# Kernel tuning notes

Hardware: AMD Instinct MI355X
Metric: run time of the kernel (lower is better)

Reference implementation:

```python
import jax, jax.numpy as jnp
import numpy as np

LN_EPS = 1e-5  # torch LayerNorm default

def _lnorm(x):
    # LayerNorm over last dim, no affine params
    mu = jnp.mean(x, axis=-1, keepdims=True)
    var = jnp.var(x, axis=-1, keepdims=True)
    return (x - mu) / jnp.sqrt(var + LN_EPS)

def setup_inputs() -> dict:
    key = jax.random.key(0)
    k0, k1, k2, k3 = jax.random.split(key, 4)
    B, S, D, H = 4, 4096, 1024, 64
    xs_q = jax.random.normal(k0, (B, S, D), dtype=jnp.float32)
    # torch Linear(D, H, bias=False) stores weight [H, D]; we store [D, H] = W.T
    sc = 1.0 / np.sqrt(D)
    Wq = jax.random.normal(k1, (D, H), dtype=jnp.float32) * sc
    Wk = jax.random.normal(k2, (D, H), dtype=jnp.float32) * sc
    Wv = jax.random.normal(k3, (D, H), dtype=jnp.float32) * sc
    return {"xs_q": xs_q, "Wq": Wq, "Wk": Wk, "Wv": Wv}

def reference(xs_q, Wq, Wk, Wv):
    # self-attention: xs_k_v = xs_q
    qs = _lnorm(jnp.einsum('bsd,dh->bsh', xs_q, Wq))  # [B,S,H]
    ks = _lnorm(jnp.einsum('bsd,dh->bsh', xs_q, Wk))
    vs = jnp.einsum('bsd,dh->bsh', xs_q, Wv)
    scaling = 1.0 / jnp.sqrt(jnp.asarray(qs.shape[-1], dtype=qs.dtype))
    att = jnp.einsum('bqh,bkh->bqk', qs, ks)          # [B,S,S] full attention matrix
    probs = jax.nn.softmax(scaling * att, axis=-1)
    vsp = jnp.einsum('bqk,bkh->bqh', probs, vs)       # [B,S,H]
    return vsp
```

## Files before the change

### kernel.cpp

```cpp
#include <hip/hip_runtime.h>
#include <hip/hip_bf16.h>


typedef __bf16 bf16x8 __attribute__((ext_vector_type(8)));
typedef __bf16 bf16x4 __attribute__((ext_vector_type(4)));
typedef short s16x4 __attribute__((ext_vector_type(4)));
typedef float f32x4 __attribute__((ext_vector_type(4)));

#define NROW 16384
#define DD   1024
#define HH   64
#define SS   4096
#define LS   68

#if __has_builtin(__builtin_amdgcn_mfma_f32_16x16x16_bf16)
#define MFMA16(a, b, c) __builtin_amdgcn_mfma_f32_16x16x16_bf16((a), (b), (c), 0, 0, 0)
#define HAVE_MFMA16 1
#elif __has_builtin(__builtin_amdgcn_mfma_f32_16x16x16bf16_1k)
#define MFMA16(a, b, c)                                             \
  __builtin_amdgcn_mfma_f32_16x16x16bf16_1k(                        \
      __builtin_bit_cast(s16x4, (a)), __builtin_bit_cast(s16x4, (b)), (c), 0, 0, 0)
#define HAVE_MFMA16 1
#endif

static __device__ inline unsigned short f2bf_u(float x) {
  __bf16 b = (__bf16)x;
  return __builtin_bit_cast(unsigned short, b);
}
static __device__ inline uint2 pk4f(float a, float b, float c, float d) {
  return make_uint2((unsigned)f2bf_u(a) | ((unsigned)f2bf_u(b) << 16),
                    (unsigned)f2bf_u(c) | ((unsigned)f2bf_u(d) << 16));
}
static __device__ inline bf16x8 ld8(const __bf16* p) {
  bf16x4 lo = *reinterpret_cast<const bf16x4*>(p);
  bf16x4 hi = *reinterpret_cast<const bf16x4*>(p + 4);
  return __builtin_shufflevector(lo, hi, 0, 1, 2, 3, 4, 5, 6, 7);
}

__global__ __launch_bounds__(256) void k_transpose_w(
    const float* __restrict__ Wq, const float* __restrict__ Wk,
    const float* __restrict__ Wv, __bf16* __restrict__ WT) {
  int idx = blockIdx.x * 256 + threadIdx.x;
  int mat = idx >> 16;
  int rem = idx & 65535;
  int k = rem >> 6, h = rem & 63;
  const float* W = (mat == 0) ? Wq : ((mat == 1) ? Wk : Wv);
  WT[(size_t)(mat * 64 + h) * DD + k] = (__bf16)W[rem];
}

__global__ __launch_bounds__(128, 2) void k_proj(
    const float* __restrict__ X, const __bf16* __restrict__ WT,
    __bf16* __restrict__ qb, __bf16* __restrict__ kbp, __bf16* __restrict__ vT) {
  __shared__ __bf16 Xs[32 * LS];
  __shared__ __bf16 Ws[192 * LS];
  const int t = threadIdx.x, lane = t & 63, w = t >> 6;
  const int quad = lane >> 4, m = lane & 15;
  const int Mb = blockIdx.x * 32;

  f32x4 acc[12];
#pragma unroll
  for (int i = 0; i < 12; i++) acc[i] = (f32x4){0.f, 0.f, 0.f, 0.f};

  float4 xr[4];
  bf16x8 wr[12];
#pragma unroll
  for (int i = 0; i < 4; i++) {
    int c = t + i * 128, row = c >> 4, col = (c & 15) * 4;
    xr[i] = *reinterpret_cast<const float4*>(&X[(size_t)(Mb + row) * DD + col]);
  }
#pragma unroll
  for (int i = 0; i < 12; i++) {
    int c = t + i * 128, row = c >> 3, col = (c & 7) * 8;
    wr[i] = *reinterpret_cast<const bf16x8*>(&WT[(size_t)row * DD + col]);
  }

  for (int s = 0; s < 16; s++) {
    if (s) __syncthreads();
#pragma unroll
    for (int i = 0; i < 4; i++) {
      int c = t + i * 128, row = c >> 4, col = (c & 15) * 4;
      *reinterpret_cast<uint2*>(&Xs[row * LS + col]) =
          pk4f(xr[i].x, xr[i].y, xr[i].z, xr[i].w);
    }
#pragma unroll
    for (int i = 0; i < 12; i++) {
      int c = t + i * 128, row = c >> 3, col = (c & 7) * 8;
      uint4 raw = __builtin_bit_cast(uint4, wr[i]);
      __bf16* wd = &Ws[row * LS + col];
      *reinterpret_cast<uint2*>(wd) = make_uint2(raw.x, raw.y);
      *reinterpret_cast<uint2*>(wd + 4) = make_uint2(raw.z, raw.w);
    }
    __syncthreads();
    if (s + 1 < 16) {
      const int ko = (s + 1) * 64;
#pragma unroll
      for (int i = 0; i < 4; i++) {
        int c = t + i * 128, row = c >> 4, col = (c & 15) * 4;
        xr[i] = *reinterpret_cast<const float4*>(
            &X[(size_t)(Mb + row) * DD + ko + col]);
      }
#pragma unroll
      for (int i = 0; i < 12; i++) {
        int c = t + i * 128, row = c >> 3, col = (c & 7) * 8;
        wr[i] = *reinterpret_cast<const bf16x8*>(
            &WT[(size_t)row * DD + ko + col]);
      }
    }
#pragma unroll
    for (int kk = 0; kk < 2; kk++) {
      bf16x8 a = ld8(&Xs[(16 * w + m) * LS + 32 * kk + quad * 8]);
#pragma unroll
      for (int nt = 0; nt < 12; nt++) {
        bf16x8 bfr = ld8(&Ws[(16 * nt + m) * LS + 32 * kk + quad * 8]);
        acc[nt] = __builtin_amdgcn_mfma_f32_16x16x32_bf16(a, bfr, acc[nt], 0, 0, 0);
      }
    }
  }

#pragma unroll
  for (int mat = 0; mat < 2; mat++) {
#pragma unroll
    for (int reg = 0; reg < 4; reg++) {
      float s = 0.f, s2 = 0.f;
#pragma unroll
      for (int ntl = 0; ntl < 4; ntl++) {
        float x = acc[mat * 4 + ntl][reg];
        s += x; s2 += x * x;
      }
#pragma unroll
      for (int off = 1; off < 16; off <<= 1) {
        s += __shfl_xor(s, off, 64);
        s2 += __shfl_xor(s2, off, 64);
      }
      float mu = s * (1.0f / 64.0f);
      float var = s2 * (1.0f / 64.0f) - mu * mu;
      float rstd = rsqrtf(var + 1e-5f);
      float scl = (mat == 0) ? 0.125f * 1.44269504f * rstd : rstd;
#pragma unroll
      for (int ntl = 0; ntl < 4; ntl++)
        acc[mat * 4 + ntl][reg] = (acc[mat * 4 + ntl][reg] - mu) * scl;
    }
  }

  const int rowbase = Mb + 16 * w + quad * 4;
#pragma unroll
  for (int nt = 0; nt < 4; nt++)
#pragma unroll
    for (int reg = 0; reg < 4; reg++) {
      qb[(size_t)(rowbase + reg) * HH + m + 16 * nt] = (__bf16)acc[nt][reg];
      kbp[(size_t)(rowbase + reg) * HH + m + 16 * nt] = (__bf16)acc[4 + nt][reg];
    }
  const int b = Mb >> 12;
  const int s0 = (Mb & 4095) + 16 * w + quad * 4;
#pragma unroll
  for (int nt = 0; nt < 4; nt++) {
    ushort4 pk = make_ushort4(f2bf_u(acc[8 + nt][0]), f2bf_u(acc[8 + nt][1]),
                              f2bf_u(acc[8 + nt][2]), f2bf_u(acc[8 + nt][3]));
    *reinterpret_cast<ushort4*>(
        &vT[((size_t)(b * 64) + m + 16 * nt) * SS + s0]) = pk;
  }
}

__global__ __launch_bounds__(256, 4) void k_attn(
    const __bf16* __restrict__ qb, const __bf16* __restrict__ kbp,
    const __bf16* __restrict__ vT, float* __restrict__ Op,
    float* __restrict__ lp, int spbits) {
  __shared__ __align__(16) char smem[17408];
  __bf16* Klds = (__bf16*)smem;
  __bf16* Vlds = (__bf16*)(smem + 8704);
  const int t = threadIdx.x, lane = t & 63, w = t >> 6;
  const int quad = lane >> 4, m = lane & 15;
  const int wq = w >> 1, wk = w & 1;
  const int nsp = 1 << spbits;
  const int qt = blockIdx.x >> spbits, sp = blockIdx.x & (nsp - 1);
  const int KPS = SS >> spbits;
  const int Mb = qt * 64;
  const int b = Mb >> 12;
  const size_t kvbase = (size_t)b * SS * HH;

  bf16x8 qf[2][2];
#pragma unroll
  for (int ntl = 0; ntl < 2; ntl++)
#pragma unroll
    for (int kk = 0; kk < 2; kk++)
      qf[ntl][kk] = *reinterpret_cast<const bf16x8*>(
          &qb[(size_t)(Mb + (2 * wq + ntl) * 16 + m) * HH + 32 * kk + quad * 8]);

  f32x4 O[4][2];
#pragma unroll
  for (int i = 0; i < 4; i++)
#pragma unroll
    for (int j = 0; j < 2; j++) O[i][j] = (f32x4){0.f, 0.f, 0.f, 0.f};
  float ll[2] = {0.f, 0.f};

  const int c0row = t >> 3, ck0 = (t & 7) * 8;
  const int c1row = c0row + 32;
  const int kb_lo = sp * KPS, kb_hi = kb_lo + KPS;

  uint4 kd0, kd1, vd0, vd1;
  kd0 = *reinterpret_cast<const uint4*>(&kbp[kvbase + (size_t)(kb_lo + c0row) * HH + ck0]);
  kd1 = *reinterpret_cast<const uint4*>(&kbp[kvbase + (size_t)(kb_lo + c1row) * HH + ck0]);
  vd0 = *reinterpret_cast<const uint4*>(&vT[(size_t)(b * 64 + c0row) * SS + kb_lo + ck0]);
  vd1 = *reinterpret_cast<const uint4*>(&vT[(size_t)(b * 64 + c1row) * SS + kb_lo + ck0]);

  for (int kb0 = kb_lo; kb0 < kb_hi; kb0 += 64) {
    {
      __bf16* kp0 = &Klds[c0row * LS + ck0];
      __bf16* kp1 = &Klds[c1row * LS + ck0];
      __bf16* vp0 = &Vlds[c0row * LS + ck0];
      __bf16* vp1 = &Vlds[c1row * LS + ck0];
      *reinterpret_cast<uint2*>(kp0) = make_uint2(kd0.x, kd0.y);
      *reinterpret_cast<uint2*>(kp0 + 4) = make_uint2(kd0.z, kd0.w);
      *reinterpret_cast<uint2*>(kp1) = make_uint2(kd1.x, kd1.y);
      *reinterpret_cast<uint2*>(kp1 + 4) = make_uint2(kd1.z, kd1.w);
      *reinterpret_cast<uint2*>(vp0) = make_uint2(vd0.x, vd0.y);
      *reinterpret_cast<uint2*>(vp0 + 4) = make_uint2(vd0.z, vd0.w);
      *reinterpret_cast<uint2*>(vp1) = make_uint2(vd1.x, vd1.y);
      *reinterpret_cast<uint2*>(vp1 + 4) = make_uint2(vd1.z, vd1.w);
    }
    __syncthreads();
    if (kb0 + 64 < kb_hi) {
      kd0 = *reinterpret_cast<const uint4*>(&kbp[kvbase + (size_t)(kb0 + 64 + c0row) * HH + ck0]);
      kd1 = *reinterpret_cast<const uint4*>(&kbp[kvbase + (size_t)(kb0 + 64 + c1row) * HH + ck0]);
      vd0 = *reinterpret_cast<const uint4*>(&vT[(size_t)(b * 64 + c0row) * SS + kb0 + 64 + ck0]);
      vd1 = *reinterpret_cast<const uint4*>(&vT[(size_t)(b * 64 + c1row) * SS + kb0 + 64 + ck0]);
    }

#pragma unroll
    for (int ktl = 0; ktl < 2; ktl++) {
      const int kt = 2 * wk + ktl;
      f32x4 sc[2];
      sc[0] = (f32x4){0.f, 0.f, 0.f, 0.f};
      sc[1] = (f32x4){0.f, 0.f, 0.f, 0.f};
#pragma unroll
      for (int kk = 0; kk < 2; kk++) {
        bf16x8 kf = ld8(&Klds[(kt * 16 + m) * LS + 32 * kk + quad * 8]);
        sc[0] = __builtin_amdgcn_mfma_f32_16x16x32_bf16(kf, qf[0][kk], sc[0], 0, 0, 0);
        sc[1] = __builtin_amdgcn_mfma_f32_16x16x32_bf16(kf, qf[1][kk], sc[1], 0, 0, 0);
      }
#pragma unroll
      for (int ntl = 0; ntl < 2; ntl++) {
        float p0 = exp2f(sc[ntl][0]), p1 = exp2f(sc[ntl][1]);
        float p2 = exp2f(sc[ntl][2]), p3 = exp2f(sc[ntl][3]);
        ll[ntl] += (p0 + p1) + (p2 + p3);
        bf16x4 pf;
        pf[0] = (__bf16)p0; pf[1] = (__bf16)p1;
        pf[2] = (__bf16)p2; pf[3] = (__bf16)p3;
#ifdef HAVE_MFMA16
#pragma unroll
        for (int ht = 0; ht < 4; ht++) {
          bf16x4 vf = *reinterpret_cast<const bf16x4*>(
              &Vlds[(16 * ht + m) * LS + kt * 16 + quad * 4]);
          O[ht][ntl] = MFMA16(vf, pf, O[ht][ntl]);
        }
#else
        uint2 pd = __builtin_bit_cast(uint2, pf);
        int lo_src = 32 * quad + m, hi_src = 32 * quad + 16 + m;
        unsigned b0 = (unsigned)__shfl((int)pd.x, lo_src, 64);
        unsigned b1 = (unsigned)__shfl((int)pd.y, lo_src, 64);
        unsigned b2 = (unsigned)__shfl((int)pd.x, hi_src, 64);
        unsigned b3 = (unsigned)__shfl((int)pd.y, hi_src, 64);
        uint4 bz = (quad < 2) ? make_uint4(b0, b1, b2, b3)
                              : make_uint4(0u, 0u, 0u, 0u);
        bf16x8 bfrag = __builtin_bit_cast(bf16x8, bz);
#pragma unroll
        for (int ht = 0; ht < 4; ht++) {
          bf16x8 vf = ld8(&Vlds[(16 * ht + m) * LS + kt * 16 + (quad & 1) * 8]);
          O[ht][ntl] =
              __builtin_amdgcn_mfma_f32_16x16x32_bf16(vf, bfrag, O[ht][ntl], 0, 0, 0);
        }
#endif
      }
    }
    __syncthreads();
  }

#pragma unroll
  for (int ntl = 0; ntl < 2; ntl++) {
    ll[ntl] += __shfl_xor(ll[ntl], 16, 64);
    ll[ntl] += __shfl_xor(ll[ntl], 32, 64);
  }

  float* obuf = (float*)smem;
  float* lbuf = (float*)(smem + 16896);
  __syncthreads();
  if (wk == 1) {
#pragma unroll
    for (int ht = 0; ht < 4; ht++)
#pragma unroll
      for (int ntl = 0; ntl < 2; ntl++)
#pragma unroll
        for (int reg = 0; reg < 4; reg++)
          obuf[wq * 2112 + (16 * ht + quad * 4 + reg) * 33 + ntl * 16 + m] =
              O[ht][ntl][reg];
    if (quad == 0) {
      lbuf[(2 * wq + 0) * 16 + m] = ll[0];
      lbuf[(2 * wq + 1) * 16 + m] = ll[1];
    }
  }
  __syncthreads();
  if (wk == 0) {
#pragma unroll
    for (int ht = 0; ht < 4; ht++)
#pragma unroll
      for (int ntl = 0; ntl < 2; ntl++)
#pragma unroll
        for (int reg = 0; reg < 4; reg++)
          O[ht][ntl][reg] +=
              obuf[wq * 2112 + (16 * ht + quad * 4 + reg) * 33 + ntl * 16 + m];
#pragma unroll
    for (int ntl = 0; ntl < 2; ntl++) {
      const int qg = Mb + (2 * wq + ntl) * 16 + m;
      ll[ntl] += lbuf[(2 * wq + ntl) * 16 + m];
#pragma unroll
      for (int ht = 0; ht < 4; ht++) {
        f32x4 v = O[ht][ntl];
        *reinterpret_cast<float4*>(
            &Op[((size_t)sp * NROW + qg) * HH + 16 * ht + 4 * quad]) =
            make_float4(v[0], v[1], v[2], v[3]);
      }
      if (quad == 0) lp[sp * NROW + qg] = ll[ntl];
    }
  }
}

__global__ __launch_bounds__(256) void k_comb(const float* __restrict__ Op,
                                              const float* __restrict__ lp,
                                              float* __restrict__ out, int nsp) {
  int idx = blockIdx.x * 256 + threadIdx.x;
  int row = idx >> 6;
  float o = 0.f, l = 0.f;
  for (int j = 0; j < nsp; j++) {
    o += Op[(size_t)j * NROW * HH + idx];
    l += lp[j * NROW + row];
  }
  out[idx] = o / l;
}

extern "C" void kernel_launch(void* const* d_in, const int* in_sizes, int n_in,
                              void* d_out, int out_size, void* d_ws, size_t ws_size,
                              hipStream_t stream) {
  const float* X  = (const float*)d_in[0];
  const float* Wq = (const float*)d_in[1];
  const float* Wk = (const float*)d_in[2];
  const float* Wv = (const float*)d_in[3];
  float* out = (float*)d_out;
  char* ws = (char*)d_ws;

  __bf16* WT  = (__bf16*)(ws);
  __bf16* qb  = (__bf16*)(ws + (size_t)512 * 1024);
  __bf16* kbp = (__bf16*)(ws + (size_t)2560 * 1024);
  __bf16* vT  = (__bf16*)(ws + (size_t)4608 * 1024);
  float*  Op  = (float*)(ws + (size_t)6656 * 1024);
  const size_t need8 = (size_t)(6656 + 8 * 4096 + 512) * 1024;
  const int spbits = (ws_size >= need8) ? 3 : 2;
  const int nsp = 1 << spbits;
  float* lp = (float*)(ws + (size_t)(6656 + nsp * 4096) * 1024);

  hipLaunchKernelGGL(k_transpose_w, dim3(768), dim3(256), 0, stream, Wq, Wk, Wv, WT);
  hipLaunchKernelGGL(k_proj, dim3(NROW / 32), dim3(128), 0, stream, X, WT, qb, kbp, vT);
  hipLaunchKernelGGL(k_attn, dim3((NROW / 64) * nsp), dim3(256), 0, stream,
                     qb, kbp, vT, Op, lp, spbits);
  hipLaunchKernelGGL(k_comb, dim3(NROW * HH / 256), dim3(256), 0, stream,
                     Op, lp, out, nsp);
}
```

Measured before the change: 160.8 us.

## Repartition warps: split-K in projection, all-keys per warp in attention

```diff
diff --git a/kernel.cpp b/kernel.cpp
--- a/kernel.cpp
+++ b/kernel.cpp
@@ -48,43 +48,46 @@
   WT[(size_t)(mat * 64 + h) * DD + k] = (__bf16)W[rem];
 }
 
-__global__ __launch_bounds__(128, 2) void k_proj(
+__global__ __launch_bounds__(256, 2) void k_proj(
     const float* __restrict__ X, const __bf16* __restrict__ WT,
     __bf16* __restrict__ qb, __bf16* __restrict__ kbp, __bf16* __restrict__ vT) {
-  __shared__ __bf16 Xs[32 * LS];
-  __shared__ __bf16 Ws[192 * LS];
+  __shared__ __align__(16) char smem[30464];
+  __bf16* Xs = (__bf16*)smem;
+  __bf16* Ws = (__bf16*)(smem + 4352);
   const int t = threadIdx.x, lane = t & 63, w = t >> 6;
   const int quad = lane >> 4, m = lane & 15;
+  const int wl = w & 1;
+  const int kh = w >> 1;
   const int Mb = blockIdx.x * 32;
 
   f32x4 acc[12];
 #pragma unroll
   for (int i = 0; i < 12; i++) acc[i] = (f32x4){0.f, 0.f, 0.f, 0.f};
 
-  float4 xr[4];
-  bf16x8 wr[12];
-#pragma unroll
-  for (int i = 0; i < 4; i++) {
-    int c = t + i * 128, row = c >> 4, col = (c & 15) * 4;
+  float4 xr[2];
+  bf16x8 wr[6];
+#pragma unroll
+  for (int i = 0; i < 2; i++) {
+    int c = t + i * 256, row = c >> 4, col = (c & 15) * 4;
     xr[i] = *reinterpret_cast<const float4*>(&X[(size_t)(Mb + row) * DD + col]);
   }
 #pragma unroll
-  for (int i = 0; i < 12; i++) {
-    int c = t + i * 128, row = c >> 3, col = (c & 7) * 8;
+  for (int i = 0; i < 6; i++) {
+    int c = t + i * 256, row = c >> 3, col = (c & 7) * 8;
     wr[i] = *reinterpret_cast<const bf16x8*>(&WT[(size_t)row * DD + col]);
   }
 
   for (int s = 0; s < 16; s++) {
     if (s) __syncthreads();
 #pragma unroll
-    for (int i = 0; i < 4; i++) {
-      int c = t + i * 128, row = c >> 4, col = (c & 15) * 4;
+    for (int i = 0; i < 2; i++) {
+      int c = t + i * 256, row = c >> 4, col = (c & 15) * 4;
       *reinterpret_cast<uint2*>(&Xs[row * LS + col]) =
           pk4f(xr[i].x, xr[i].y, xr[i].z, xr[i].w);
     }
 #pragma unroll
-    for (int i = 0; i < 12; i++) {
-      int c = t + i * 128, row = c >> 3, col = (c & 7) * 8;
+    for (int i = 0; i < 6; i++) {
+      int c = t + i * 256, row = c >> 3, col = (c & 7) * 8;
       uint4 raw = __builtin_bit_cast(uint4, wr[i]);
       __bf16* wd = &Ws[row * LS + col];
       *reinterpret_cast<uint2*>(wd) = make_uint2(raw.x, raw.y);
@@ -94,28 +97,38 @@
     if (s + 1 < 16) {
       const int ko = (s + 1) * 64;
 #pragma unroll
-      for (int i = 0; i < 4; i++) {
-        int c = t + i * 128, row = c >> 4, col = (c & 15) * 4;
+      for (int i = 0; i < 2; i++) {
+        int c = t + i * 256, row = c >> 4, col = (c & 15) * 4;
         xr[i] = *reinterpret_cast<const float4*>(
             &X[(size_t)(Mb + row) * DD + ko + col]);
       }
 #pragma unroll
-      for (int i = 0; i < 12; i++) {
-        int c = t + i * 128, row = c >> 3, col = (c & 7) * 8;
+      for (int i = 0; i < 6; i++) {
+        int c = t + i * 256, row = c >> 3, col = (c & 7) * 8;
         wr[i] = *reinterpret_cast<const bf16x8*>(
             &WT[(size_t)row * DD + ko + col]);
       }
     }
-#pragma unroll
-    for (int kk = 0; kk < 2; kk++) {
-      bf16x8 a = ld8(&Xs[(16 * w + m) * LS + 32 * kk + quad * 8]);
-#pragma unroll
-      for (int nt = 0; nt < 12; nt++) {
-        bf16x8 bfr = ld8(&Ws[(16 * nt + m) * LS + 32 * kk + quad * 8]);
-        acc[nt] = __builtin_amdgcn_mfma_f32_16x16x32_bf16(a, bfr, acc[nt], 0, 0, 0);
-      }
-    }
-  }
+    bf16x8 a = ld8(&Xs[(16 * wl + m) * LS + 32 * kh + quad * 8]);
+#pragma unroll
+    for (int nt = 0; nt < 12; nt++) {
+      bf16x8 bfr = ld8(&Ws[(16 * nt + m) * LS + 32 * kh + quad * 8]);
+      acc[nt] = __builtin_amdgcn_mfma_f32_16x16x32_bf16(a, bfr, acc[nt], 0, 0, 0);
+    }
+  }
+
+  __syncthreads();
+  float* red = (float*)smem;
+  if (kh == 1) {
+#pragma unroll
+    for (int nt = 0; nt < 12; nt++)
+      *reinterpret_cast<f32x4*>(&red[(wl * 64 + lane) * 52 + nt * 4]) = acc[nt];
+  }
+  __syncthreads();
+  if (kh == 1) return;
+#pragma unroll
+  for (int nt = 0; nt < 12; nt++)
+    acc[nt] += *reinterpret_cast<const f32x4*>(&red[(wl * 64 + lane) * 52 + nt * 4]);
 
 #pragma unroll
   for (int mat = 0; mat < 2; mat++) {
@@ -142,7 +155,7 @@
     }
   }
 
-  const int rowbase = Mb + 16 * w + quad * 4;
+  const int rowbase = Mb + 16 * wl + quad * 4;
 #pragma unroll
   for (int nt = 0; nt < 4; nt++)
 #pragma unroll
@@ -151,7 +164,7 @@
       kbp[(size_t)(rowbase + reg) * HH + m + 16 * nt] = (__bf16)acc[4 + nt][reg];
     }
   const int b = Mb >> 12;
-  const int s0 = (Mb & 4095) + 16 * w + quad * 4;
+  const int s0 = (Mb & 4095) + 16 * wl + quad * 4;
 #pragma unroll
   for (int nt = 0; nt < 4; nt++) {
     ushort4 pk = make_ushort4(f2bf_u(acc[8 + nt][0]), f2bf_u(acc[8 + nt][1]),
@@ -170,11 +183,10 @@
   __bf16* Vlds = (__bf16*)(smem + 8704);
   const int t = threadIdx.x, lane = t & 63, w = t >> 6;
   const int quad = lane >> 4, m = lane & 15;
-  const int wq = w >> 1, wk = w & 1;
   const int nsp = 1 << spbits;
   const int qt = blockIdx.x >> spbits, sp = blockIdx.x & (nsp - 1);
   const int KPS = SS >> spbits;
-  const int Mb = qt * 64;
+  const int Mb = qt * 128;
   const int b = Mb >> 12;
   const size_t kvbase = (size_t)b * SS * HH;
 
@@ -184,7 +196,7 @@
 #pragma unroll
     for (int kk = 0; kk < 2; kk++)
       qf[ntl][kk] = *reinterpret_cast<const bf16x8*>(
-          &qb[(size_t)(Mb + (2 * wq + ntl) * 16 + m) * HH + 32 * kk + quad * 8]);
+          &qb[(size_t)(Mb + 32 * w + 16 * ntl + m) * HH + 32 * kk + quad * 8]);
 
   f32x4 O[4][2];
 #pragma unroll
@@ -227,34 +239,38 @@
     }
 
 #pragma unroll
-    for (int ktl = 0; ktl < 2; ktl++) {
-      const int kt = 2 * wk + ktl;
+    for (int ktl = 0; ktl < 4; ktl++) {
+      bf16x8 kf0 = ld8(&Klds[(ktl * 16 + m) * LS + quad * 8]);
+      bf16x8 kf1 = ld8(&Klds[(ktl * 16 + m) * LS + 32 + quad * 8]);
       f32x4 sc[2];
       sc[0] = (f32x4){0.f, 0.f, 0.f, 0.f};
       sc[1] = (f32x4){0.f, 0.f, 0.f, 0.f};
 #pragma unroll
-      for (int kk = 0; kk < 2; kk++) {
-        bf16x8 kf = ld8(&Klds[(kt * 16 + m) * LS + 32 * kk + quad * 8]);
-        sc[0] = __builtin_amdgcn_mfma_f32_16x16x32_bf16(kf, qf[0][kk], sc[0], 0, 0, 0);
-        sc[1] = __builtin_amdgcn_mfma_f32_16x16x32_bf16(kf, qf[1][kk], sc[1], 0, 0, 0);
-      }
+      for (int ntl = 0; ntl < 2; ntl++) {
+        sc[ntl] = __builtin_amdgcn_mfma_f32_16x16x32_bf16(kf0, qf[ntl][0], sc[ntl], 0, 0, 0);
+        sc[ntl] = __builtin_amdgcn_mfma_f32_16x16x32_bf16(kf1, qf[ntl][1], sc[ntl], 0, 0, 0);
+      }
+      bf16x4 pf[2];
 #pragma unroll
       for (int ntl = 0; ntl < 2; ntl++) {
         float p0 = exp2f(sc[ntl][0]), p1 = exp2f(sc[ntl][1]);
         float p2 = exp2f(sc[ntl][2]), p3 = exp2f(sc[ntl][3]);
         ll[ntl] += (p0 + p1) + (p2 + p3);
-        bf16x4 pf;
-        pf[0] = (__bf16)p0; pf[1] = (__bf16)p1;
-        pf[2] = (__bf16)p2; pf[3] = (__bf16)p3;
+        pf[ntl][0] = (__bf16)p0; pf[ntl][1] = (__bf16)p1;
+        pf[ntl][2] = (__bf16)p2; pf[ntl][3] = (__bf16)p3;
+      }
 #ifdef HAVE_MFMA16
 #pragma unroll
-        for (int ht = 0; ht < 4; ht++) {
-          bf16x4 vf = *reinterpret_cast<const bf16x4*>(
-              &Vlds[(16 * ht + m) * LS + kt * 16 + quad * 4]);
-          O[ht][ntl] = MFMA16(vf, pf, O[ht][ntl]);
-        }
+      for (int ht = 0; ht < 4; ht++) {
+        bf16x4 vf = *reinterpret_cast<const bf16x4*>(
+            &Vlds[(16 * ht + m) * LS + ktl * 16 + quad * 4]);
+        O[ht][0] = MFMA16(vf, pf[0], O[ht][0]);
+        O[ht][1] = MFMA16(vf, pf[1], O[ht][1]);
+      }
 #else
-        uint2 pd = __builtin_bit_cast(uint2, pf);
+#pragma unroll
+      for (int ntl = 0; ntl < 2; ntl++) {
+        uint2 pd = __builtin_bit_cast(uint2, pf[ntl]);
         int lo_src = 32 * quad + m, hi_src = 32 * quad + 16 + m;
         unsigned b0 = (unsigned)__shfl((int)pd.x, lo_src, 64);
         unsigned b1 = (unsigned)__shfl((int)pd.y, lo_src, 64);
@@ -265,12 +281,12 @@
         bf16x8 bfrag = __builtin_bit_cast(bf16x8, bz);
 #pragma unroll
         for (int ht = 0; ht < 4; ht++) {
-          bf16x8 vf = ld8(&Vlds[(16 * ht + m) * LS + kt * 16 + (quad & 1) * 8]);
+          bf16x8 vf = ld8(&Vlds[(16 * ht + m) * LS + ktl * 16 + (quad & 1) * 8]);
           O[ht][ntl] =
               __builtin_amdgcn_mfma_f32_16x16x32_bf16(vf, bfrag, O[ht][ntl], 0, 0, 0);
         }
+      }
 #endif
-      }
     }
     __syncthreads();
   }
@@ -281,46 +297,17 @@
     ll[ntl] += __shfl_xor(ll[ntl], 32, 64);
   }
 
-  float* obuf = (float*)smem;
-  float* lbuf = (float*)(smem + 16896);
-  __syncthreads();
-  if (wk == 1) {
-#pragma unroll
-    for (int ht = 0; ht < 4; ht++)
-#pragma unroll
-      for (int ntl = 0; ntl < 2; ntl++)
-#pragma unroll
-        for (int reg = 0; reg < 4; reg++)
-          obuf[wq * 2112 + (16 * ht + quad * 4 + reg) * 33 + ntl * 16 + m] =
-              O[ht][ntl][reg];
-    if (quad == 0) {
-      lbuf[(2 * wq + 0) * 16 + m] = ll[0];
-      lbuf[(2 * wq + 1) * 16 + m] = ll[1];
-    }
-  }
-  __syncthreads();
-  if (wk == 0) {
-#pragma unroll
-    for (int ht = 0; ht < 4; ht++)
-#pragma unroll
-      for (int ntl = 0; ntl < 2; ntl++)
-#pragma unroll
-        for (int reg = 0; reg < 4; reg++)
-          O[ht][ntl][reg] +=
-              obuf[wq * 2112 + (16 * ht + quad * 4 + reg) * 33 + ntl * 16 + m];
-#pragma unroll
-    for (int ntl = 0; ntl < 2; ntl++) {
-      const int qg = Mb + (2 * wq + ntl) * 16 + m;
-      ll[ntl] += lbuf[(2 * wq + ntl) * 16 + m];
-#pragma unroll
-      for (int ht = 0; ht < 4; ht++) {
-        f32x4 v = O[ht][ntl];
-        *reinterpret_cast<float4*>(
-            &Op[((size_t)sp * NROW + qg) * HH + 16 * ht + 4 * quad]) =
-            make_float4(v[0], v[1], v[2], v[3]);
-      }
-      if (quad == 0) lp[sp * NROW + qg] = ll[ntl];
-    }
+#pragma unroll
+  for (int ntl = 0; ntl < 2; ntl++) {
+    const int qg = Mb + 32 * w + 16 * ntl + m;
+#pragma unroll
+    for (int ht = 0; ht < 4; ht++) {
+      f32x4 v = O[ht][ntl];
+      *reinterpret_cast<float4*>(
+          &Op[((size_t)sp * NROW + qg) * HH + 16 * ht + 4 * quad]) =
+          make_float4(v[0], v[1], v[2], v[3]);
+    }
+    if (quad == 0) lp[sp * NROW + qg] = ll[ntl];
   }
 }
 
@@ -358,8 +345,8 @@
   float* lp = (float*)(ws + (size_t)(6656 + nsp * 4096) * 1024);
 
   hipLaunchKernelGGL(k_transpose_w, dim3(768), dim3(256), 0, stream, Wq, Wk, Wv, WT);
-  hipLaunchKernelGGL(k_proj, dim3(NROW / 32), dim3(128), 0, stream, X, WT, qb, kbp, vT);
-  hipLaunchKernelGGL(k_attn, dim3((NROW / 64) * nsp), dim3(256), 0, stream,
+  hipLaunchKernelGGL(k_proj, dim3(NROW / 32), dim3(256), 0, stream, X, WT, qb, kbp, vT);
+  hipLaunchKernelGGL(k_attn, dim3((NROW / 128) * nsp), dim3(256), 0, stream,
                      qb, kbp, vT, Op, lp, spbits);
   hipLaunchKernelGGL(k_comb, dim3(NROW * HH / 256), dim3(256), 0, stream,
                      Op, lp, out, nsp);
```

Result: slower. 179.9 us (+11.9%).

## Retile projection by output column per wave and double KV tile in attention

Applied to the files above, without the earlier changes.

```diff
diff --git a/kernel.cpp b/kernel.cpp
--- a/kernel.cpp
+++ b/kernel.cpp
@@ -12,6 +12,7 @@
 #define HH   64
 #define SS   4096
 #define LS   68
+#define VS2  132
 
 #if __has_builtin(__builtin_amdgcn_mfma_f32_16x16x16_bf16)
 #define MFMA16(a, b, c) __builtin_amdgcn_mfma_f32_16x16x16_bf16((a), (b), (c), 0, 0, 0)
@@ -51,20 +52,20 @@
 __global__ __launch_bounds__(128, 2) void k_proj(
     const float* __restrict__ X, const __bf16* __restrict__ WT,
     __bf16* __restrict__ qb, __bf16* __restrict__ kbp, __bf16* __restrict__ vT) {
-  __shared__ __bf16 Xs[32 * LS];
+  __shared__ __bf16 Xs[16 * LS];
   __shared__ __bf16 Ws[192 * LS];
   const int t = threadIdx.x, lane = t & 63, w = t >> 6;
   const int quad = lane >> 4, m = lane & 15;
-  const int Mb = blockIdx.x * 32;
-
-  f32x4 acc[12];
-#pragma unroll
-  for (int i = 0; i < 12; i++) acc[i] = (f32x4){0.f, 0.f, 0.f, 0.f};
-
-  float4 xr[4];
+  const int Mb = blockIdx.x * 16;
+
+  f32x4 acc[6];
+#pragma unroll
+  for (int i = 0; i < 6; i++) acc[i] = (f32x4){0.f, 0.f, 0.f, 0.f};
+
+  float4 xr[2];
   bf16x8 wr[12];
 #pragma unroll
-  for (int i = 0; i < 4; i++) {
+  for (int i = 0; i < 2; i++) {
     int c = t + i * 128, row = c >> 4, col = (c & 15) * 4;
     xr[i] = *reinterpret_cast<const float4*>(&X[(size_t)(Mb + row) * DD + col]);
   }
@@ -77,7 +78,7 @@
   for (int s = 0; s < 16; s++) {
     if (s) __syncthreads();
 #pragma unroll
-    for (int i = 0; i < 4; i++) {
+    for (int i = 0; i < 2; i++) {
       int c = t + i * 128, row = c >> 4, col = (c & 15) * 4;
       *reinterpret_cast<uint2*>(&Xs[row * LS + col]) =
           pk4f(xr[i].x, xr[i].y, xr[i].z, xr[i].w);
@@ -94,7 +95,7 @@
     if (s + 1 < 16) {
       const int ko = (s + 1) * 64;
 #pragma unroll
-      for (int i = 0; i < 4; i++) {
+      for (int i = 0; i < 2; i++) {
         int c = t + i * 128, row = c >> 4, col = (c & 15) * 4;
         xr[i] = *reinterpret_cast<const float4*>(
             &X[(size_t)(Mb + row) * DD + ko + col]);
@@ -108,56 +109,55 @@
     }
 #pragma unroll
     for (int kk = 0; kk < 2; kk++) {
-      bf16x8 a = ld8(&Xs[(16 * w + m) * LS + 32 * kk + quad * 8]);
-#pragma unroll
-      for (int nt = 0; nt < 12; nt++) {
+      bf16x8 a = ld8(&Xs[m * LS + 32 * kk + quad * 8]);
+#pragma unroll
+      for (int j = 0; j < 6; j++) {
+        const int nt = (j < 4) ? (4 * w + j) : (8 + 2 * w + (j - 4));
         bf16x8 bfr = ld8(&Ws[(16 * nt + m) * LS + 32 * kk + quad * 8]);
-        acc[nt] = __builtin_amdgcn_mfma_f32_16x16x32_bf16(a, bfr, acc[nt], 0, 0, 0);
-      }
-    }
-  }
-
-#pragma unroll
-  for (int mat = 0; mat < 2; mat++) {
-#pragma unroll
-    for (int reg = 0; reg < 4; reg++) {
-      float s = 0.f, s2 = 0.f;
-#pragma unroll
-      for (int ntl = 0; ntl < 4; ntl++) {
-        float x = acc[mat * 4 + ntl][reg];
-        s += x; s2 += x * x;
-      }
-#pragma unroll
-      for (int off = 1; off < 16; off <<= 1) {
-        s += __shfl_xor(s, off, 64);
-        s2 += __shfl_xor(s2, off, 64);
-      }
-      float mu = s * (1.0f / 64.0f);
-      float var = s2 * (1.0f / 64.0f) - mu * mu;
-      float rstd = rsqrtf(var + 1e-5f);
-      float scl = (mat == 0) ? 0.125f * 1.44269504f * rstd : rstd;
-#pragma unroll
-      for (int ntl = 0; ntl < 4; ntl++)
-        acc[mat * 4 + ntl][reg] = (acc[mat * 4 + ntl][reg] - mu) * scl;
-    }
-  }
-
-  const int rowbase = Mb + 16 * w + quad * 4;
+        acc[j] = __builtin_amdgcn_mfma_f32_16x16x32_bf16(a, bfr, acc[j], 0, 0, 0);
+      }
+    }
+  }
+
+  const float lnscl_base = (w == 0) ? 0.125f * 1.44269504f : 1.0f;
+#pragma unroll
+  for (int reg = 0; reg < 4; reg++) {
+    float s = 0.f, s2 = 0.f;
+#pragma unroll
+    for (int ntl = 0; ntl < 4; ntl++) {
+      float x = acc[ntl][reg];
+      s += x; s2 += x * x;
+    }
+#pragma unroll
+    for (int off = 1; off < 16; off <<= 1) {
+      s += __shfl_xor(s, off, 64);
+      s2 += __shfl_xor(s2, off, 64);
+    }
+    float mu = s * (1.0f / 64.0f);
+    float var = s2 * (1.0f / 64.0f) - mu * mu;
+    float rstd = rsqrtf(var + 1e-5f);
+    float scl = lnscl_base * rstd;
+#pragma unroll
+    for (int ntl = 0; ntl < 4; ntl++)
+      acc[ntl][reg] = (acc[ntl][reg] - mu) * scl;
+  }
+
+  __bf16* dst = (w == 0) ? qb : kbp;
+  const int rowbase = Mb + quad * 4;
 #pragma unroll
   for (int nt = 0; nt < 4; nt++)
 #pragma unroll
-    for (int reg = 0; reg < 4; reg++) {
-      qb[(size_t)(rowbase + reg) * HH + m + 16 * nt] = (__bf16)acc[nt][reg];
-      kbp[(size_t)(rowbase + reg) * HH + m + 16 * nt] = (__bf16)acc[4 + nt][reg];
-    }
+    for (int reg = 0; reg < 4; reg++)
+      dst[(size_t)(rowbase + reg) * HH + m + 16 * nt] = (__bf16)acc[nt][reg];
+
   const int b = Mb >> 12;
-  const int s0 = (Mb & 4095) + 16 * w + quad * 4;
-#pragma unroll
-  for (int nt = 0; nt < 4; nt++) {
-    ushort4 pk = make_ushort4(f2bf_u(acc[8 + nt][0]), f2bf_u(acc[8 + nt][1]),
-                              f2bf_u(acc[8 + nt][2]), f2bf_u(acc[8 + nt][3]));
+  const int s0 = (Mb & 4095) + quad * 4;
+#pragma unroll
+  for (int j = 0; j < 2; j++) {
+    ushort4 pk = make_ushort4(f2bf_u(acc[4 + j][0]), f2bf_u(acc[4 + j][1]),
+                              f2bf_u(acc[4 + j][2]), f2bf_u(acc[4 + j][3]));
     *reinterpret_cast<ushort4*>(
-        &vT[((size_t)(b * 64) + m + 16 * nt) * SS + s0]) = pk;
+        &vT[((size_t)(b * 64) + m + 16 * (2 * w + j)) * SS + s0]) = pk;
   }
 }
 
@@ -165,9 +165,9 @@
     const __bf16* __restrict__ qb, const __bf16* __restrict__ kbp,
     const __bf16* __restrict__ vT, float* __restrict__ Op,
     float* __restrict__ lp, int spbits) {
-  __shared__ __align__(16) char smem[17408];
+  __shared__ __align__(16) char smem[34304];
   __bf16* Klds = (__bf16*)smem;
-  __bf16* Vlds = (__bf16*)(smem + 8704);
+  __bf16* Vlds = (__bf16*)(smem + 17408);
   const int t = threadIdx.x, lane = t & 63, w = t >> 6;
   const int quad = lane >> 4, m = lane & 15;
   const int wq = w >> 1, wk = w & 1;
@@ -193,42 +193,43 @@
     for (int j = 0; j < 2; j++) O[i][j] = (f32x4){0.f, 0.f, 0.f, 0.f};
   float ll[2] = {0.f, 0.f};
 
-  const int c0row = t >> 3, ck0 = (t & 7) * 8;
-  const int c1row = c0row + 32;
+  const int kcr = t >> 3, kcc = (t & 7) * 8;
+  const int vcr = t >> 4, vcc = (t & 15) * 8;
   const int kb_lo = sp * KPS, kb_hi = kb_lo + KPS;
 
-  uint4 kd0, kd1, vd0, vd1;
-  kd0 = *reinterpret_cast<const uint4*>(&kbp[kvbase + (size_t)(kb_lo + c0row) * HH + ck0]);
-  kd1 = *reinterpret_cast<const uint4*>(&kbp[kvbase + (size_t)(kb_lo + c1row) * HH + ck0]);
-  vd0 = *reinterpret_cast<const uint4*>(&vT[(size_t)(b * 64 + c0row) * SS + kb_lo + ck0]);
-  vd1 = *reinterpret_cast<const uint4*>(&vT[(size_t)(b * 64 + c1row) * SS + kb_lo + ck0]);
-
-  for (int kb0 = kb_lo; kb0 < kb_hi; kb0 += 64) {
-    {
-      __bf16* kp0 = &Klds[c0row * LS + ck0];
-      __bf16* kp1 = &Klds[c1row * LS + ck0];
-      __bf16* vp0 = &Vlds[c0row * LS + ck0];
-      __bf16* vp1 = &Vlds[c1row * LS + ck0];
-      *reinterpret_cast<uint2*>(kp0) = make_uint2(kd0.x, kd0.y);
-      *reinterpret_cast<uint2*>(kp0 + 4) = make_uint2(kd0.z, kd0.w);
-      *reinterpret_cast<uint2*>(kp1) = make_uint2(kd1.x, kd1.y);
-      *reinterpret_cast<uint2*>(kp1 + 4) = make_uint2(kd1.z, kd1.w);
-      *reinterpret_cast<uint2*>(vp0) = make_uint2(vd0.x, vd0.y);
-      *reinterpret_cast<uint2*>(vp0 + 4) = make_uint2(vd0.z, vd0.w);
-      *reinterpret_cast<uint2*>(vp1) = make_uint2(vd1.x, vd1.y);
-      *reinterpret_cast<uint2*>(vp1 + 4) = make_uint2(vd1.z, vd1.w);
+  uint4 kd[4], vd[4];
+#pragma unroll
+  for (int i = 0; i < 4; i++) {
+    kd[i] = *reinterpret_cast<const uint4*>(
+        &kbp[kvbase + (size_t)(kb_lo + kcr + 32 * i) * HH + kcc]);
+    vd[i] = *reinterpret_cast<const uint4*>(
+        &vT[(size_t)(b * 64 + vcr + 16 * i) * SS + kb_lo + vcc]);
+  }
+
+  for (int kb0 = kb_lo; kb0 < kb_hi; kb0 += 128) {
+#pragma unroll
+    for (int i = 0; i < 4; i++) {
+      __bf16* kp = &Klds[(kcr + 32 * i) * LS + kcc];
+      __bf16* vp = &Vlds[(vcr + 16 * i) * VS2 + vcc];
+      *reinterpret_cast<uint2*>(kp) = make_uint2(kd[i].x, kd[i].y);
+      *reinterpret_cast<uint2*>(kp + 4) = make_uint2(kd[i].z, kd[i].w);
+      *reinterpret_cast<uint2*>(vp) = make_uint2(vd[i].x, vd[i].y);
+      *reinterpret_cast<uint2*>(vp + 4) = make_uint2(vd[i].z, vd[i].w);
     }
     __syncthreads();
-    if (kb0 + 64 < kb_hi) {
-      kd0 = *reinterpret_cast<const uint4*>(&kbp[kvbase + (size_t)(kb0 + 64 + c0row) * HH + ck0]);
-      kd1 = *reinterpret_cast<const uint4*>(&kbp[kvbase + (size_t)(kb0 + 64 + c1row) * HH + ck0]);
-      vd0 = *reinterpret_cast<const uint4*>(&vT[(size_t)(b * 64 + c0row) * SS + kb0 + 64 + ck0]);
-      vd1 = *reinterpret_cast<const uint4*>(&vT[(size_t)(b * 64 + c1row) * SS + kb0 + 64 + ck0]);
-    }
-
-#pragma unroll
-    for (int ktl = 0; ktl < 2; ktl++) {
-      const int kt = 2 * wk + ktl;
+    if (kb0 + 128 < kb_hi) {
+#pragma unroll
+      for (int i = 0; i < 4; i++) {
+        kd[i] = *reinterpret_cast<const uint4*>(
+            &kbp[kvbase + (size_t)(kb0 + 128 + kcr + 32 * i) * HH + kcc]);
+        vd[i] = *reinterpret_cast<const uint4*>(
+            &vT[(size_t)(b * 64 + vcr + 16 * i) * SS + kb0 + 128 + vcc]);
+      }
+    }
+
+#pragma unroll
+    for (int ktl = 0; ktl < 4; ktl++) {
+      const int kt = 4 * wk + ktl;
       f32x4 sc[2];
       sc[0] = (f32x4){0.f, 0.f, 0.f, 0.f};
       sc[1] = (f32x4){0.f, 0.f, 0.f, 0.f};
@@ -250,7 +251,7 @@
 #pragma unroll
         for (int ht = 0; ht < 4; ht++) {
           bf16x4 vf = *reinterpret_cast<const bf16x4*>(
-              &Vlds[(16 * ht + m) * LS + kt * 16 + quad * 4]);
+              &Vlds[(16 * ht + m) * VS2 + kt * 16 + quad * 4]);
           O[ht][ntl] = MFMA16(vf, pf, O[ht][ntl]);
         }
 #else
@@ -265,7 +266,7 @@
         bf16x8 bfrag = __builtin_bit_cast(bf16x8, bz);
 #pragma unroll
         for (int ht = 0; ht < 4; ht++) {
-          bf16x8 vf = ld8(&Vlds[(16 * ht + m) * LS + kt * 16 + (quad & 1) * 8]);
+          bf16x8 vf = ld8(&Vlds[(16 * ht + m) * VS2 + kt * 16 + (quad & 1) * 8]);
           O[ht][ntl] =
               __builtin_amdgcn_mfma_f32_16x16x32_bf16(vf, bfrag, O[ht][ntl], 0, 0, 0);
         }
@@ -352,13 +353,12 @@
   __bf16* kbp = (__bf16*)(ws + (size_t)2560 * 1024);
   __bf16* vT  = (__bf16*)(ws + (size_t)4608 * 1024);
   float*  Op  = (float*)(ws + (size_t)6656 * 1024);
-  const size_t need8 = (size_t)(6656 + 8 * 4096 + 512) * 1024;
-  const int spbits = (ws_size >= need8) ? 3 : 2;
+  const int spbits = 2;
   const int nsp = 1 << spbits;
   float* lp = (float*)(ws + (size_t)(6656 + nsp * 4096) * 1024);
 
   hipLaunchKernelGGL(k_transpose_w, dim3(768), dim3(256), 0, stream, Wq, Wk, Wv, WT);
-  hipLaunchKernelGGL(k_proj, dim3(NROW / 32), dim3(128), 0, stream, X, WT, qb, kbp, vT);
+  hipLaunchKernelGGL(k_proj, dim3(NROW / 16), dim3(128), 0, stream, X, WT, qb, kbp, vT);
   hipLaunchKernelGGL(k_attn, dim3((NROW / 64) * nsp), dim3(256), 0, stream,
                      qb, kbp, vT, Op, lp, spbits);
   hipLaunchKernelGGL(k_comb, dim3(NROW * HH / 256), dim3(256), 0, stream,
```

After: 171.3 us. 6.5% more time.

## Fuse split-K combine into attention kernel via last-block atomic counter

Applied to the files above, without the earlier changes.

```diff
diff --git a/kernel.cpp b/kernel.cpp
--- a/kernel.cpp
+++ b/kernel.cpp
@@ -164,8 +164,10 @@
 __global__ __launch_bounds__(256, 4) void k_attn(
     const __bf16* __restrict__ qb, const __bf16* __restrict__ kbp,
     const __bf16* __restrict__ vT, float* __restrict__ Op,
-    float* __restrict__ lp, int spbits) {
+    float* __restrict__ lp, int* __restrict__ cnt,
+    float* __restrict__ out, int spbits) {
   __shared__ __align__(16) char smem[17408];
+  __shared__ int lastflag;
   __bf16* Klds = (__bf16*)smem;
   __bf16* Vlds = (__bf16*)(smem + 8704);
   const int t = threadIdx.x, lane = t & 63, w = t >> 6;
@@ -322,19 +324,27 @@
       if (quad == 0) lp[sp * NROW + qg] = ll[ntl];
     }
   }
-}
-
-__global__ __launch_bounds__(256) void k_comb(const float* __restrict__ Op,
-                                              const float* __restrict__ lp,
-                                              float* __restrict__ out, int nsp) {
-  int idx = blockIdx.x * 256 + threadIdx.x;
-  int row = idx >> 6;
-  float o = 0.f, l = 0.f;
-  for (int j = 0; j < nsp; j++) {
-    o += Op[(size_t)j * NROW * HH + idx];
-    l += lp[j * NROW + row];
-  }
-  out[idx] = o / l;
+
+  __threadfence();
+  __syncthreads();
+  if (t == 0) {
+    int old = atomicAdd(&cnt[qt], 1);
+    lastflag = (old == nsp - 1);
+  }
+  __syncthreads();
+  if (lastflag) {
+    __threadfence();
+    for (int i = t; i < 64 * HH; i += 256) {
+      int row = i >> 6;
+      int qg = Mb + row;
+      float o = 0.f, l = 0.f;
+      for (int j = 0; j < nsp; j++) {
+        o += Op[((size_t)j * NROW + qg) * HH + (i & 63)];
+        l += lp[j * NROW + qg];
+      }
+      out[(size_t)qg * HH + (i & 63)] = o / l;
+    }
+  }
 }
 
 extern "C" void kernel_launch(void* const* d_in, const int* in_sizes, int n_in,
@@ -352,15 +362,14 @@
   __bf16* kbp = (__bf16*)(ws + (size_t)2560 * 1024);
   __bf16* vT  = (__bf16*)(ws + (size_t)4608 * 1024);
   float*  Op  = (float*)(ws + (size_t)6656 * 1024);
-  const size_t need8 = (size_t)(6656 + 8 * 4096 + 512) * 1024;
-  const int spbits = (ws_size >= need8) ? 3 : 2;
+  const int spbits = 2;
   const int nsp = 1 << spbits;
   float* lp = (float*)(ws + (size_t)(6656 + nsp * 4096) * 1024);
+  int* cnt = (int*)(ws + (size_t)(6656 + nsp * 4096 + 256) * 1024);
 
   hipLaunchKernelGGL(k_transpose_w, dim3(768), dim3(256), 0, stream, Wq, Wk, Wv, WT);
   hipLaunchKernelGGL(k_proj, dim3(NROW / 32), dim3(128), 0, stream, X, WT, qb, kbp, vT);
+  hipMemsetAsync(cnt, 0, 1024, stream);
   hipLaunchKernelGGL(k_attn, dim3((NROW / 64) * nsp), dim3(256), 0, stream,
-                     qb, kbp, vT, Op, lp, spbits);
-  hipLaunchKernelGGL(k_comb, dim3(NROW * HH / 256), dim3(256), 0, stream,
-                     Op, lp, out, nsp);
-}
+                     qb, kbp, vT, Op, lp, cnt, out, spbits);
+}
```

New measurement: 338.0 us. 2.1x slower.
